# Performance work log

Measured on AMD Instinct MI355X. Metric: run time of the kernel, lower is better.

Reference implementation:

```python
import jax, jax.numpy as jnp
import numpy as np

N, E, G = 100000, 1600000, 256
F_IN, HID, NCLS = 16, 64, 2
EPS = 1e-5


def segment_mean(v, seg, num_segments):
    s = jax.ops.segment_sum(v, seg, num_segments=num_segments)
    c = jax.ops.segment_sum(jnp.ones((v.shape[0], 1), v.dtype), seg, num_segments=num_segments)
    return s / jnp.maximum(c, 1.0)


def graph_norm(x, seg, weight, bias, mean_scale):
    # PyG GraphNorm: per-graph mean/var with learnable mean_scale
    mean = segment_mean(x, seg, G)                      # [G, C]
    centered = x - mean_scale * mean[seg]               # [N, C]
    var = segment_mean(centered * centered, seg, G)     # [G, C]
    return weight * centered * jax.lax.rsqrt(var[seg] + EPS) + bias


def gcn_conv(x, W, b, row, col, n):
    # PyG GCNConv: h = x @ W; symmetric norm with added self-loops; scatter-add; + bias
    h = x @ W                                           # [N, C_out]
    deg = jnp.zeros((n,), x.dtype).at[row].add(1.0) + 1.0  # +1 self-loop
    dinv = jax.lax.rsqrt(deg)
    norm = (dinv[row] * dinv[col])[:, None]             # [E, 1]
    agg = jnp.zeros_like(h).at[row].add(norm * h[col])  # neighbor messages
    agg = agg + (dinv * dinv)[:, None] * h              # self-loop messages
    return agg + b


def setup_inputs():
    key = jax.random.key(0)
    ks = jax.random.split(key, 16)
    x = jax.random.normal(ks[0], (N, F_IN), jnp.float32)
    edge_index = jax.random.randint(ks[1], (2, E), 0, N, jnp.int32)
    batch = jnp.sort(jax.random.randint(ks[2], (N,), 0, G, jnp.int32))
    s = lambda k, shp: jax.random.normal(k, shp, jnp.float32) * 0.05
    return {
        "x": x, "edge_index": edge_index, "batch": batch,
        "gn0_w": jnp.ones((F_IN,)), "gn0_b": jnp.zeros((F_IN,)), "gn0_ms": jnp.ones((F_IN,)),
        "W1": s(ks[3], (F_IN, HID)), "b1": jnp.zeros((HID,)),
        "gn1_w": jnp.ones((HID,)), "gn1_b": jnp.zeros((HID,)), "gn1_ms": jnp.ones((HID,)),
        "W2": s(ks[4], (HID, HID)), "b2": jnp.zeros((HID,)),
        "gn2_w": jnp.ones((HID,)), "gn2_b": jnp.zeros((HID,)), "gn2_ms": jnp.ones((HID,)),
        "W3": s(ks[5], (HID, HID)), "b3": jnp.zeros((HID,)),
        "Wd": s(ks[6], (HID, HID)), "bd": jnp.zeros((HID,)),
        "Wo": s(ks[7], (HID, NCLS)), "bo": jnp.zeros((NCLS,)),
    }


def reference(x, edge_index, batch, gn0_w, gn0_b, gn0_ms, W1, b1, gn1_w, gn1_b, gn1_ms,
              W2, b2, gn2_w, gn2_b, gn2_ms, W3, b3, Wd, bd, Wo, bo):
    row, col = edge_index[0], edge_index[1]
    h = graph_norm(x, batch, gn0_w, gn0_b, gn0_ms)
    h = jax.nn.relu(gcn_conv(h, W1, b1, row, col, N))
    h = graph_norm(h, batch, gn1_w, gn1_b, gn1_ms)
    h = jax.nn.relu(gcn_conv(h, W2, b2, row, col, N))
    h = graph_norm(h, batch, gn2_w, gn2_b, gn2_ms)
    h = jax.nn.relu(gcn_conv(h, W3, b3, row, col, N))
    g = segment_mean(h, batch, G)                       # global_mean_pool -> [G, HID]
    # dropout is identity in eval mode
    g = jax.nn.relu(g @ Wd + bd)
    logits = g @ Wo + bo
    return jax.nn.softmax(logits, axis=1)
```

## Files before the change

kernel.cpp:

```cpp
#include <hip/hip_runtime.h>
#include <hip/hip_bf16.h>

#define NN 100000
#define NE 1600000
#define NG 256
#define FIN 16
#define HID 64
#define NBK 391
#define NTILE 391
#define PMAX 4864
#define BMAXP 5632
#define MAXT (NN / 16 + NG)

__device__ __forceinline__ int lower_bound_i(const int* __restrict__ b, int n, int v) {
    int lo = 0, hi = n;
    while (lo < hi) { int m = (lo + hi) >> 1; if (b[m] < v) lo = m + 1; else hi = m; }
    return lo;
}

__device__ __forceinline__ unsigned pack_bf16(float a, float b) {
    unsigned ua = __float_as_uint(a), ub = __float_as_uint(b);
    ua = (ua + 0x7fffu + ((ua >> 16) & 1u)) >> 16;
    ub = (ub + 0x7fffu + ((ub >> 16) & 1u)) & 0xffff0000u;
    return ua | ub;
}
#define BF_LO(u) __uint_as_float((u) << 16)
#define BF_HI(u) __uint_as_float((u) & 0xffff0000u)

typedef __attribute__((ext_vector_type(8))) short bf16x8;
typedef __attribute__((ext_vector_type(4))) float f32x4;
union FU { uint4 u; bf16x8 v; };

__global__ __launch_bounds__(512) void k_bhist(const int4* __restrict__ row4, int* __restrict__ bhist) {
    __shared__ int h[NBK];
    for (int i = threadIdx.x; i < NBK; i += 512) h[i] = 0;
    __syncthreads();
    int t0 = blockIdx.x * 1024 + threadIdx.x;
#pragma unroll
    for (int it = 0; it < 2; ++it) {
        int t = t0 + it * 512;
        if (t < NE / 4) {
            int4 r = row4[t];
            atomicAdd(&h[r.x >> 8], 1); atomicAdd(&h[r.y >> 8], 1);
            atomicAdd(&h[r.z >> 8], 1); atomicAdd(&h[r.w >> 8], 1);
        }
    }
    __syncthreads();
    for (int i = threadIdx.x; i < NBK; i += 512)
        if (h[i]) atomicAdd(&bhist[i], h[i]);
}

__global__ __launch_bounds__(512) void k_bscan(const int* __restrict__ bhist, int* __restrict__ bbase,
                                               int* __restrict__ bcur) {
    __shared__ int sc[512];
    int t = threadIdx.x;
    int v = (t < NBK) ? bhist[t] : 0;
    sc[t] = v;
    __syncthreads();
    int acc = v;
    for (int off = 1; off < 512; off <<= 1) {
        int add = (t >= off) ? sc[t - off] : 0;
        __syncthreads();
        acc += add;
        sc[t] = acc;
        __syncthreads();
    }
    if (t < NBK) { bbase[t] = acc - v; bcur[t] = acc - v; }
    if (t == NBK - 1) bbase[NBK] = acc;
}

__global__ __launch_bounds__(512) void k_bscatter(const int4* __restrict__ row4, const int4* __restrict__ col4,
                                                  int* __restrict__ bcur, int2* __restrict__ pairs) {
    __shared__ int lh[NBK], lofs[NBK], lbase[NBK], lc[NBK];
    __shared__ int sc[512];
    __shared__ int2 stg[4096];
    for (int i = threadIdx.x; i < NBK; i += 512) { lh[i] = 0; lc[i] = 0; }
    __syncthreads();
    int t0 = blockIdx.x * 1024 + threadIdx.x;
#pragma unroll
    for (int it = 0; it < 2; ++it) {
        int t = t0 + it * 512;
        if (t < NE / 4) {
            int4 r = row4[t];
            atomicAdd(&lh[r.x >> 8], 1); atomicAdd(&lh[r.y >> 8], 1);
            atomicAdd(&lh[r.z >> 8], 1); atomicAdd(&lh[r.w >> 8], 1);
        }
    }
    __syncthreads();
    {
        int t = threadIdx.x;
        int v = (t < NBK) ? lh[t] : 0;
        sc[t] = v;
        __syncthreads();
        int acc = v;
        for (int off = 1; off < 512; off <<= 1) {
            int add = (t >= off) ? sc[t - off] : 0;
            __syncthreads();
            acc += add;
            sc[t] = acc;
            __syncthreads();
        }
        if (t < NBK) lofs[t] = acc - v;
    }
    if (threadIdx.x < NBK) {
        int c = lh[threadIdx.x];
        lbase[threadIdx.x] = c ? atomicAdd(&bcur[threadIdx.x], c) : 0;
    }
    __syncthreads();
#pragma unroll
    for (int it = 0; it < 2; ++it) {
        int t = t0 + it * 512;
        if (t < NE / 4) {
            int4 r = row4[t];
            int4 c = col4[t];
            int b, rk;
            b = r.x >> 8; rk = atomicAdd(&lc[b], 1); stg[lofs[b] + rk] = make_int2(r.x, c.x);
            b = r.y >> 8; rk = atomicAdd(&lc[b], 1); stg[lofs[b] + rk] = make_int2(r.y, c.y);
            b = r.z >> 8; rk = atomicAdd(&lc[b], 1); stg[lofs[b] + rk] = make_int2(r.z, c.z);
            b = r.w >> 8; rk = atomicAdd(&lc[b], 1); stg[lofs[b] + rk] = make_int2(r.w, c.w);
        }
    }
    __syncthreads();
    int nv = min(4096, NE - blockIdx.x * 4096);
    for (int j = threadIdx.x; j < nv; j += 512) {
        int2 p = stg[j];
        int b = p.x >> 8;
        pairs[lbase[b] + (j - lofs[b])] = p;
    }
}

__global__ __launch_bounds__(256) void k_bsort(const int2* __restrict__ pairs, const int* __restrict__ bbase,
                                               int* __restrict__ csr_col, int* __restrict__ startv,
                                               int* __restrict__ degc, float* __restrict__ dinv) {
    __shared__ int colo[BMAXP];
    __shared__ int cnt[256], pofs[256], c2[256], sc[256];
    int b = blockIdx.x;
    int s = bbase[b];
    int n = min(bbase[b + 1] - s, PMAX);
    cnt[threadIdx.x] = 0;
    c2[threadIdx.x] = 0;
    __syncthreads();
    for (int i = threadIdx.x; i < n; i += 256)
        atomicAdd(&cnt[pairs[s + i].x & 255], 1);
    __syncthreads();
    int c = cnt[threadIdx.x];
    int pc = (c + 3) & ~3;
    {
        int t = threadIdx.x, v = pc;
        sc[t] = v;
        __syncthreads();
        int acc = v;
        for (int off = 1; off < 256; off <<= 1) {
            int add = (t >= off) ? sc[t - off] : 0;
            __syncthreads();
            acc += add;
            sc[t] = acc;
            __syncthreads();
        }
        pofs[t] = acc - v;
    }
    __syncthreads();
    int ptot = sc[255];
    for (int i = threadIdx.x; i < ptot; i += 256) colo[i] = NN;
    __syncthreads();
    for (int i = threadIdx.x; i < n; i += 256) {
        int2 p = pairs[s + i];
        int lr = p.x & 255;
        int rk = atomicAdd(&c2[lr], 1);
        colo[pofs[lr] + rk] = p.y;
    }
    __syncthreads();
    int gb = b * BMAXP;
    for (int i = threadIdx.x; i < ptot; i += 256) csr_col[gb + i] = colo[i];
    int r = (b << 8) + threadIdx.x;
    if (r < NN) {
        startv[r] = gb + pofs[threadIdx.x];
        degc[r] = pc;
        dinv[r] = rsqrtf((float)(c + 1));
    }
}

__global__ __launch_bounds__(256) void k_setup(const int* __restrict__ batch, int* __restrict__ ntot,
                                               int* __restrict__ tg, int* __restrict__ tbase,
                                               int* __restrict__ tcnt, const float* __restrict__ W1,
                                               unsigned* __restrict__ Wt1p, unsigned* __restrict__ xb,
                                               unsigned* __restrict__ h2) {
    if (blockIdx.x == 1) {
        int t = threadIdx.x;
        int j = t >> 2, kq = t & 3;
#pragma unroll
        for (int i = 0; i < 4; i++) {
            int idx = kq * 4 + i;
            int k = idx * 2;
            unsigned v = 0;
            if (k < FIN) v = pack_bf16(W1[k * 64 + j], W1[(k + 1) * 64 + j]);
            Wt1p[j * 16 + idx] = v;
        }
        if (t < 32) h2[(long)NN * 32 + t] = 0u;
        if (t < 8) xb[(long)NN * 8 + t] = 0u;
        return;
    }
    __shared__ int gst[NG + 1];
    __shared__ int sc[NG];
    int t = threadIdx.x;
    gst[t] = lower_bound_i(batch, NN, t);
    if (t == 0) gst[NG] = NN;
    __syncthreads();
    int ng = gst[t + 1] - gst[t];
    int nt = (ng + 15) >> 4;
    sc[t] = nt;
    __syncthreads();
    int acc = nt;
    for (int off = 1; off < NG; off <<= 1) {
        int add = (t >= off) ? sc[t - off] : 0;
        __syncthreads();
        acc += add;
        sc[t] = acc;
        __syncthreads();
    }
    int ofs = acc - nt;
    for (int i = 0; i < nt; i++) {
        tg[ofs + i] = t;
        tbase[ofs + i] = gst[t] + i * 16;
        tcnt[ofs + i] = min(16, ng - i * 16);
    }
    if (t == NG - 1) ntot[0] = acc;
}

__global__ __launch_bounds__(512) void k_graphnorm16(const float* __restrict__ x, const int* __restrict__ batch,
                              const float* __restrict__ w, const float* __restrict__ b,
                              const float* __restrict__ ms, const float* __restrict__ dinv,
                              unsigned* __restrict__ xb) {
    constexpr int C = FIN, NPB = 512 / C;
    __shared__ float red[NPB][C], red2[NPB][C];
    __shared__ float mm_s[C], rs_s[C];
    int g = blockIdx.x;
    int s = lower_bound_i(batch, NN, g);
    int e = lower_bound_i(batch, NN, g + 1);
    float fc = (float)max(e - s, 1);
    int c = threadIdx.x % C, slot = threadIdx.x / C;

    float a1 = 0.f, a2 = 0.f;
    for (int i = s + slot; i < e; i += NPB) { float v = x[i * C + c]; a1 += v; a2 += v * v; }
    red[slot][c] = a1;
    red2[slot][c] = a2;
    __syncthreads();
    if (threadIdx.x < C) {
        float t1 = 0.f, t2 = 0.f;
        for (int k = 0; k < NPB; k++) { t1 += red[k][threadIdx.x]; t2 += red2[k][threadIdx.x]; }
        float mean = t1 / fc;
        float mm = ms[threadIdx.x] * mean;
        float var = t2 / fc - 2.f * mm * mean + mm * mm;
        mm_s[threadIdx.x] = mm;
        rs_s[threadIdx.x] = rsqrtf(var + 1e-5f);
    }
    __syncthreads();
    float mm = mm_s[c], ww = w[c] * rs_s[c], bb = b[c];
    for (int i = s + slot; i < e; i += NPB) {
        float v = (ww * (x[i * C + c] - mm) + bb) * dinv[i];
        float partner = __shfl_xor(v, 1);
        if ((c & 1) == 0) xb[(long)i * 8 + (c >> 1)] = pack_bf16(v, partner);
    }
}

__global__ __launch_bounds__(512) void k_gnstats2(const unsigned* __restrict__ xw, const int* __restrict__ batch,
                          const float* __restrict__ w, const float* __restrict__ b,
                          const float* __restrict__ ms, const float* __restrict__ W,
                          unsigned* __restrict__ Wtp, float* __restrict__ bias2) {
    __shared__ float4 red[16][32];
    __shared__ float sA[64], sB[64];
    int g = blockIdx.x;
    int s = lower_bound_i(batch, NN, g);
    int e = lower_bound_i(batch, NN, g + 1);
    float fc = (float)max(e - s, 1);
    int cu = threadIdx.x & 31, slot = threadIdx.x >> 5;

    float s1l = 0.f, s1h = 0.f, s2l = 0.f, s2h = 0.f;
    for (int i = s + slot; i < e; i += 16) {
        unsigned u = xw[(long)i * 32 + cu];
        float lo = BF_LO(u), hi = BF_HI(u);
        s1l += lo; s1h += hi; s2l += lo * lo; s2h += hi * hi;
    }
    red[slot][cu] = make_float4(s1l, s1h, s2l, s2h);
    __syncthreads();
    if (threadIdx.x < 64) {
        int cc = threadIdx.x, iu = cc >> 1, hi = cc & 1;
        float t1 = 0.f, t2 = 0.f;
        for (int k = 0; k < 16; k++) {
            float4 v = red[k][iu];
            t1 += hi ? v.y : v.x;
            t2 += hi ? v.w : v.z;
        }
        float mean = t1 / fc;
        float mm = ms[cc] * mean;
        float var = t2 / fc - 2.f * mm * mean + mm * mm;
        float A = w[cc] * rsqrtf(var + 1e-5f);
        sA[cc] = A;
        sB[cc] = b[cc] - A * mm;
    }
    __syncthreads();
    if (threadIdx.x < 256) {
        int j = threadIdx.x >> 2, kq = threadIdx.x & 3;
        unsigned* wrow = Wtp + ((long)g * 64 + j) * 32 + kq * 8;
        float part = 0.f;
#pragma unroll
        for (int i = 0; i < 8; i++) {
            int k = kq * 16 + 2 * i;
            float w0 = W[k * 64 + j], w1 = W[(k + 1) * 64 + j];
            wrow[i] = pack_bf16(sA[k] * w0, sA[k + 1] * w1);
            part += sB[k] * w0 + sB[k + 1] * w1;
        }
        part += __shfl_xor(part, 1);
        part += __shfl_xor(part, 2);
        if (kq == 0) bias2[g * 64 + j] = part;
    }
}

__global__ __launch_bounds__(256) void k_gather16(const unsigned* __restrict__ xb, const int* __restrict__ startv,
                           const int* __restrict__ degc, const float* __restrict__ dinv,
                           const int* __restrict__ csr_col, unsigned* __restrict__ agg) {
    int wave = (blockIdx.x * blockDim.x + threadIdx.x) >> 6;
    if (wave >= NN) return;
    int lane = threadIdx.x & 63;
    unsigned p = lane & 7;
    int g = lane >> 3;
    int s = startv[wave], pcnt = degc[wave];
    float di = dinv[wave];
    float ax = 0.f, ay = 0.f;
    int k = g;
    for (; k + 8 < pcnt; k += 16) {
        unsigned c0 = (unsigned)csr_col[s + k], c1 = (unsigned)csr_col[s + k + 8];
        unsigned u0 = xb[c0 * 8u + p], u1 = xb[c1 * 8u + p];
        ax += BF_LO(u0) + BF_LO(u1);
        ay += BF_HI(u0) + BF_HI(u1);
    }
    if (k < pcnt) {
        unsigned c0 = (unsigned)csr_col[s + k];
        unsigned u0 = xb[c0 * 8u + p];
        ax += BF_LO(u0);
        ay += BF_HI(u0);
    }
    ax += __shfl_xor(ax, 8);  ay += __shfl_xor(ay, 8);
    ax += __shfl_xor(ax, 16); ay += __shfl_xor(ay, 16);
    ax += __shfl_xor(ax, 32); ay += __shfl_xor(ay, 32);
    if (g == 0) {
        unsigned u = xb[(unsigned)wave * 8u + p];
        ax = (ax + BF_LO(u)) * di;
        ay = (ay + BF_HI(u)) * di;
        agg[(long)wave * 16 + p] = pack_bf16(ax, ay);
    } else if (g == 1) {
        agg[(long)wave * 16 + 8 + p] = 0u;
    }
}

template <int KU, bool PERG, bool RELU, bool DINV>
__global__ __launch_bounds__(256) void k_gemmT(const unsigned* __restrict__ Ain, const unsigned* __restrict__ Wt,
                        const float* __restrict__ biasv, const float* __restrict__ dinv,
                        const int* __restrict__ ntot, const int* __restrict__ tg,
                        const int* __restrict__ tbase, const int* __restrict__ tcnt,
                        unsigned* __restrict__ Aout) {
    const int RW = KU * 16;
    int tix = blockIdx.x * 4 + (threadIdx.x >> 6);
    if (tix >= ntot[0]) return;
    int g = tg[tix], base = tbase[tix], n = tcnt[tix];
    int l = threadIdx.x & 63, r = l & 15, q = l >> 4;
    FU a[KU];
#pragma unroll
    for (int s = 0; s < KU; s++) {
        if (r < n) a[s].u = *(const uint4*)(Ain + (long)(base + r) * RW + s * 16 + q * 4);
        else a[s].u = make_uint4(0, 0, 0, 0);
    }
    const unsigned* wb = PERG ? (Wt + (long)g * 64 * RW) : Wt;
    f32x4 acc[4];
#pragma unroll
    for (int t = 0; t < 4; t++) {
        acc[t] = (f32x4){0.f, 0.f, 0.f, 0.f};
#pragma unroll
        for (int s = 0; s < KU; s++) {
            FU bfrag;
            bfrag.u = *(const uint4*)(wb + (long)(t * 16 + r) * RW + s * 16 + q * 4);
            acc[t] = __builtin_amdgcn_mfma_f32_16x16x32_bf16(a[s].v, bfrag.v, acc[t], 0, 0, 0);
        }
    }
    const float* bb = PERG ? (biasv + g * 64) : biasv;
    float dv[4];
#pragma unroll
    for (int e = 0; e < 4; e++) {
        int node = base + q * 4 + e;
        dv[e] = DINV ? ((node < NN) ? dinv[node] : 0.f) : 1.f;
    }
#pragma unroll
    for (int t = 0; t < 4; t++) {
        float bv = bb[t * 16 + r];
#pragma unroll
        for (int e = 0; e < 4; e++) {
            float v = acc[t][e] + bv;
            if (RELU) v = fmaxf(v, 0.f);
            if (DINV) v *= dv[e];
            float part = __shfl_xor(v, 1);
            if ((q * 4 + e) < n && (r & 1) == 0)
                Aout[(long)(base + q * 4 + e) * 32 + t * 8 + (r >> 1)] = pack_bf16(v, part);
        }
    }
}

__global__ __launch_bounds__(256) void k_gather64(const unsigned* __restrict__ h2, const int* __restrict__ startv,
                           const int* __restrict__ degc, const float* __restrict__ dinv,
                           const int* __restrict__ csr_col, const float* __restrict__ bias,
                           unsigned* __restrict__ outp) {
    int wave = (blockIdx.x * blockDim.x + threadIdx.x) >> 6;
    if (wave >= NN) return;
    int lane = threadIdx.x & 63;
    unsigned p = lane & 31;
    int g = lane >> 5;
    int s = startv[wave], pcnt = degc[wave];
    float di = dinv[wave];
    float ax = 0.f, ay = 0.f;
    if (g == 0) {
        unsigned u = h2[(unsigned)wave * 32u + p];
        ax = BF_LO(u);
        ay = BF_HI(u);
    }
    int k = g * 8;
    for (; k + 8 <= pcnt; k += 16) {
        uint4 c0 = *(const uint4*)(csr_col + s + k);
        uint4 c1 = *(const uint4*)(csr_col + s + k + 4);
        unsigned u0 = h2[c0.x * 32u + p], u1 = h2[c0.y * 32u + p],
                 u2 = h2[c0.z * 32u + p], u3 = h2[c0.w * 32u + p],
                 u4 = h2[c1.x * 32u + p], u5 = h2[c1.y * 32u + p],
                 u6 = h2[c1.z * 32u + p], u7 = h2[c1.w * 32u + p];
        ax += BF_LO(u0) + BF_LO(u1) + BF_LO(u2) + BF_LO(u3)
            + BF_LO(u4) + BF_LO(u5) + BF_LO(u6) + BF_LO(u7);
        ay += BF_HI(u0) + BF_HI(u1) + BF_HI(u2) + BF_HI(u3)
            + BF_HI(u4) + BF_HI(u5) + BF_HI(u6) + BF_HI(u7);
    }
    if (k < pcnt) {
        uint4 c0 = *(const uint4*)(csr_col + s + k);
        unsigned u0 = h2[c0.x * 32u + p], u1 = h2[c0.y * 32u + p],
                 u2 = h2[c0.z * 32u + p], u3 = h2[c0.w * 32u + p];
        ax += BF_LO(u0) + BF_LO(u1) + BF_LO(u2) + BF_LO(u3);
        ay += BF_HI(u0) + BF_HI(u1) + BF_HI(u2) + BF_HI(u3);
    }
    ax += __shfl_xor(ax, 32);
    ay += __shfl_xor(ay, 32);
    if (g == 0) {
        float2 bv = ((const float2*)bias)[p];
        float vx = fmaxf(ax * di + bv.x, 0.f);
        float vy = fmaxf(ay * di + bv.y, 0.f);
        outp[(unsigned)wave * 32u + p] = pack_bf16(vx, vy);
    }
}

__global__ __launch_bounds__(1024) void k_poolhead(const unsigned* __restrict__ xw, const int* __restrict__ batch,
                       const float* __restrict__ Wd, const float* __restrict__ bd,
                       const float* __restrict__ Wo, const float* __restrict__ bo,
                       float* __restrict__ out) {
    __shared__ float red[16][64];
    __shared__ float wds[64 * 64];
    __shared__ float gs[64];
    int g = blockIdx.x;
    int s = lower_bound_i(batch, NN, g);
    int e = lower_bound_i(batch, NN, g + 1);
    int c = threadIdx.x & 63, slot = threadIdx.x >> 6;
    for (int i = threadIdx.x; i < 64 * 64; i += 1024) wds[i] = Wd[i];
    float acc = 0.f;
    for (int i = s + slot; i < e; i += 16) {
        unsigned u = xw[(long)i * 32 + (c >> 1)];
        acc += (c & 1) ? BF_HI(u) : BF_LO(u);
    }
    red[slot][c] = acc;
    __syncthreads();
    if (threadIdx.x < 64) {
        float t = 0.f;
        for (int k = 0; k < 16; k++) t += red[k][threadIdx.x];
        gs[threadIdx.x] = t / (float)max(e - s, 1);
    }
    __syncthreads();
    if (threadIdx.x < 64) {
        int j = threadIdx.x;
        float a2 = bd[j];
        for (int k = 0; k < 64; k++) a2 += gs[k] * wds[k * 64 + j];
        float hv = fmaxf(a2, 0.f);
        float p0 = hv * Wo[j * 2 + 0], p1 = hv * Wo[j * 2 + 1];
        for (int off = 32; off; off >>= 1) { p0 += __shfl_down(p0, off); p1 += __shfl_down(p1, off); }
        if (j == 0) {
            float l0 = p0 + bo[0], l1 = p1 + bo[1];
            float m = fmaxf(l0, l1);
            float e0 = expf(l0 - m), e1 = expf(l1 - m);
            float inv = 1.f / (e0 + e1);
            out[g * 2 + 0] = e0 * inv;
            out[g * 2 + 1] = e1 * inv;
        }
    }
}

extern "C" void kernel_launch(void* const* d_in, const int* in_sizes, int n_in,
                              void* d_out, int out_size, void* d_ws, size_t ws_size,
                              hipStream_t stream) {
    const float* x = (const float*)d_in[0];
    const int* ei = (const int*)d_in[1];
    const int* row = ei;
    const int* col = ei + NE;
    const int* batch = (const int*)d_in[2];
    const float* gn0w = (const float*)d_in[3];
    const float* gn0b = (const float*)d_in[4];
    const float* gn0ms = (const float*)d_in[5];
    const float* W1 = (const float*)d_in[6];
    const float* b1 = (const float*)d_in[7];
    const float* gn1w = (const float*)d_in[8];
    const float* gn1b = (const float*)d_in[9];
    const float* gn1ms = (const float*)d_in[10];
    const float* W2 = (const float*)d_in[11];
    const float* b2 = (const float*)d_in[12];
    const float* gn2w = (const float*)d_in[13];
    const float* gn2b = (const float*)d_in[14];
    const float* gn2ms = (const float*)d_in[15];
    const float* W3 = (const float*)d_in[16];
    const float* b3 = (const float*)d_in[17];
    const float* Wd = (const float*)d_in[18];
    const float* bd = (const float*)d_in[19];
    const float* Wo = (const float*)d_in[20];
    const float* bo = (const float*)d_in[21];
    float* outp = (float*)d_out;

    int* bhist = (int*)d_ws;
    int* bbase = bhist + 512;
    int* bcur = bbase + 512;
    int* startv = bcur + 512;
    int* degc = startv + NN;
    float* dinv = (float*)(degc + NN);
    int* csr_col = (int*)(dinv + NN);
    int* ntot = csr_col + (long)NBK * BMAXP;
    int* tg = ntot + 16;
    int* tbase = tg + 6608;
    int* tcnt = tbase + 6608;
    unsigned* Wt1p = (unsigned*)(tcnt + 6608);
    unsigned* Wtp = Wt1p + 1024;
    float* bias2 = (float*)(Wtp + (long)NG * 64 * 32);
    unsigned* xb = (unsigned*)(bias2 + NG * 64);
    unsigned* agg16 = xb + (long)NN * 8 + 16;
    unsigned* bufA = agg16 + (long)NN * 16;
    unsigned* bufB = bufA + (long)NN * 32;
    unsigned* h2 = bufB + (long)NN * 32;
    int2* pairs = (int2*)bufA;

    const int NBG = (MAXT + 3) / 4;

    hipMemsetAsync(bhist, 0, 512 * sizeof(int), stream);
    k_bhist<<<NTILE, 512, 0, stream>>>((const int4*)row, bhist);
    k_bscan<<<1, 512, 0, stream>>>(bhist, bbase, bcur);
    k_bscatter<<<NTILE, 512, 0, stream>>>((const int4*)row, (const int4*)col, bcur, pairs);
    k_bsort<<<NBK, 256, 0, stream>>>(pairs, bbase, csr_col, startv, degc, dinv);

    k_setup<<<2, 256, 0, stream>>>(batch, ntot, tg, tbase, tcnt, W1, Wt1p, xb, h2);

    k_graphnorm16<<<NG, 512, 0, stream>>>(x, batch, gn0w, gn0b, gn0ms, dinv, xb);
    k_gather16<<<(NN * 64 + 255) / 256, 256, 0, stream>>>(xb, startv, degc, dinv, csr_col, agg16);
    k_gemmT<1, false, true, false><<<NBG, 256, 0, stream>>>(agg16, Wt1p, b1, dinv, ntot, tg, tbase, tcnt, bufA);

    k_gnstats2<<<NG, 512, 0, stream>>>(bufA, batch, gn1w, gn1b, gn1ms, W2, Wtp, bias2);
    k_gemmT<2, true, false, true><<<NBG, 256, 0, stream>>>(bufA, Wtp, bias2, dinv, ntot, tg, tbase, tcnt, h2);
    k_gather64<<<(NN * 64 + 255) / 256, 256, 0, stream>>>(h2, startv, degc, dinv, csr_col, b2, bufB);

    k_gnstats2<<<NG, 512, 0, stream>>>(bufB, batch, gn2w, gn2b, gn2ms, W3, Wtp, bias2);
    k_gemmT<2, true, false, true><<<NBG, 256, 0, stream>>>(bufB, Wtp, bias2, dinv, ntot, tg, tbase, tcnt, h2);
    k_gather64<<<(NN * 64 + 255) / 256, 256, 0, stream>>>(h2, startv, degc, dinv, csr_col, b3, bufA);

    k_poolhead<<<NG, 1024, 0, stream>>>(bufA, batch, Wd, bd, Wo, bo, outp);
}
```

Baseline: 382.3 us.

## Drop bucket histogram and scan passes by using fixed-capacity bucket slots

The global bucket histogram and scan kernels are removed. Each bucket now gets a fixed slot of BMAXP pairs, and k_bscatter reserves positions with an atomic counter (bcur), which k_bsort then reads as that bucket's count. This saves two kernel launches and one full read of the row array, but relies on no bucket exceeding its fixed capacity. Per-row degrees are no longer padded to multiples of four, so the 64-wide gather switches from aligned uint4 column loads to bounds-checked scalar loads.

Measured after the change: 375.9 us. About the same (-1.7%).

```diff
diff --git a/kernel.cpp b/kernel.cpp
--- a/kernel.cpp
+++ b/kernel.cpp
@@ -30,44 +30,6 @@
 typedef __attribute__((ext_vector_type(8))) short bf16x8;
 typedef __attribute__((ext_vector_type(4))) float f32x4;
 union FU { uint4 u; bf16x8 v; };
-
-__global__ __launch_bounds__(512) void k_bhist(const int4* __restrict__ row4, int* __restrict__ bhist) {
-    __shared__ int h[NBK];
-    for (int i = threadIdx.x; i < NBK; i += 512) h[i] = 0;
-    __syncthreads();
-    int t0 = blockIdx.x * 1024 + threadIdx.x;
-#pragma unroll
-    for (int it = 0; it < 2; ++it) {
-        int t = t0 + it * 512;
-        if (t < NE / 4) {
-            int4 r = row4[t];
-            atomicAdd(&h[r.x >> 8], 1); atomicAdd(&h[r.y >> 8], 1);
-            atomicAdd(&h[r.z >> 8], 1); atomicAdd(&h[r.w >> 8], 1);
-        }
-    }
-    __syncthreads();
-    for (int i = threadIdx.x; i < NBK; i += 512)
-        if (h[i]) atomicAdd(&bhist[i], h[i]);
-}
-
-__global__ __launch_bounds__(512) void k_bscan(const int* __restrict__ bhist, int* __restrict__ bbase,
-                                               int* __restrict__ bcur) {
-    __shared__ int sc[512];
-    int t = threadIdx.x;
-    int v = (t < NBK) ? bhist[t] : 0;
-    sc[t] = v;
-    __syncthreads();
-    int acc = v;
-    for (int off = 1; off < 512; off <<= 1) {
-        int add = (t >= off) ? sc[t - off] : 0;
-        __syncthreads();
-        acc += add;
-        sc[t] = acc;
-        __syncthreads();
-    }
-    if (t < NBK) { bbase[t] = acc - v; bcur[t] = acc - v; }
-    if (t == NBK - 1) bbase[NBK] = acc;
-}
 
 __global__ __launch_bounds__(512) void k_bscatter(const int4* __restrict__ row4, const int4* __restrict__ col4,
                                                   int* __restrict__ bcur, int2* __restrict__ pairs) {
@@ -125,23 +87,23 @@
     for (int j = threadIdx.x; j < nv; j += 512) {
         int2 p = stg[j];
         int b = p.x >> 8;
-        pairs[lbase[b] + (j - lofs[b])] = p;
-    }
-}
-
-__global__ __launch_bounds__(256) void k_bsort(const int2* __restrict__ pairs, const int* __restrict__ bbase,
+        pairs[(long)b * BMAXP + lbase[b] + (j - lofs[b])] = p;
+    }
+}
+
+__global__ __launch_bounds__(256) void k_bsort(const int2* __restrict__ pairs, const int* __restrict__ bcur,
                                                int* __restrict__ csr_col, int* __restrict__ startv,
                                                int* __restrict__ degc, float* __restrict__ dinv) {
     __shared__ int colo[BMAXP];
     __shared__ int cnt[256], pofs[256], c2[256], sc[256];
     int b = blockIdx.x;
-    int s = bbase[b];
-    int n = min(bbase[b + 1] - s, PMAX);
+    long sp = (long)b * BMAXP;
+    int n = min(bcur[b], PMAX);
     cnt[threadIdx.x] = 0;
     c2[threadIdx.x] = 0;
     __syncthreads();
     for (int i = threadIdx.x; i < n; i += 256)
-        atomicAdd(&cnt[pairs[s + i].x & 255], 1);
+        atomicAdd(&cnt[pairs[sp + i].x & 255], 1);
     __syncthreads();
     int c = cnt[threadIdx.x];
     int pc = (c + 3) & ~3;
@@ -164,7 +126,7 @@
     for (int i = threadIdx.x; i < ptot; i += 256) colo[i] = NN;
     __syncthreads();
     for (int i = threadIdx.x; i < n; i += 256) {
-        int2 p = pairs[s + i];
+        int2 p = pairs[sp + i];
         int lr = p.x & 255;
         int rk = atomicAdd(&c2[lr], 1);
         colo[pofs[lr] + rk] = p.y;
@@ -175,7 +137,7 @@
     int r = (b << 8) + threadIdx.x;
     if (r < NN) {
         startv[r] = gb + pofs[threadIdx.x];
-        degc[r] = pc;
+        degc[r] = c;
         dinv[r] = rsqrtf((float)(c + 1));
     }
 }
@@ -324,17 +286,17 @@
     int lane = threadIdx.x & 63;
     unsigned p = lane & 7;
     int g = lane >> 3;
-    int s = startv[wave], pcnt = degc[wave];
+    int s = startv[wave], cnt = degc[wave];
     float di = dinv[wave];
     float ax = 0.f, ay = 0.f;
     int k = g;
-    for (; k + 8 < pcnt; k += 16) {
+    for (; k + 8 < cnt; k += 16) {
         unsigned c0 = (unsigned)csr_col[s + k], c1 = (unsigned)csr_col[s + k + 8];
         unsigned u0 = xb[c0 * 8u + p], u1 = xb[c1 * 8u + p];
         ax += BF_LO(u0) + BF_LO(u1);
         ay += BF_HI(u0) + BF_HI(u1);
     }
-    if (k < pcnt) {
+    if (k < cnt) {
         unsigned c0 = (unsigned)csr_col[s + k];
         unsigned u0 = xb[c0 * 8u + p];
         ax += BF_LO(u0);
@@ -413,7 +375,7 @@
     int lane = threadIdx.x & 63;
     unsigned p = lane & 31;
     int g = lane >> 5;
-    int s = startv[wave], pcnt = degc[wave];
+    int s = startv[wave], cnt = degc[wave];
     float di = dinv[wave];
     float ax = 0.f, ay = 0.f;
     if (g == 0) {
@@ -421,25 +383,19 @@
         ax = BF_LO(u);
         ay = BF_HI(u);
     }
-    int k = g * 8;
-    for (; k + 8 <= pcnt; k += 16) {
-        uint4 c0 = *(const uint4*)(csr_col + s + k);
-        uint4 c1 = *(const uint4*)(csr_col + s + k + 4);
-        unsigned u0 = h2[c0.x * 32u + p], u1 = h2[c0.y * 32u + p],
-                 u2 = h2[c0.z * 32u + p], u3 = h2[c0.w * 32u + p],
-                 u4 = h2[c1.x * 32u + p], u5 = h2[c1.y * 32u + p],
-                 u6 = h2[c1.z * 32u + p], u7 = h2[c1.w * 32u + p];
-        ax += BF_LO(u0) + BF_LO(u1) + BF_LO(u2) + BF_LO(u3)
-            + BF_LO(u4) + BF_LO(u5) + BF_LO(u6) + BF_LO(u7);
-        ay += BF_HI(u0) + BF_HI(u1) + BF_HI(u2) + BF_HI(u3)
-            + BF_HI(u4) + BF_HI(u5) + BF_HI(u6) + BF_HI(u7);
-    }
-    if (k < pcnt) {
-        uint4 c0 = *(const uint4*)(csr_col + s + k);
-        unsigned u0 = h2[c0.x * 32u + p], u1 = h2[c0.y * 32u + p],
-                 u2 = h2[c0.z * 32u + p], u3 = h2[c0.w * 32u + p];
-        ax += BF_LO(u0) + BF_LO(u1) + BF_LO(u2) + BF_LO(u3);
-        ay += BF_HI(u0) + BF_HI(u1) + BF_HI(u2) + BF_HI(u3);
+    for (int k = g * 8; k < cnt; k += 16) {
+        int cc[8];
+#pragma unroll
+        for (int i = 0; i < 8; i++) {
+            int idx = k + i;
+            cc[i] = (idx < cnt) ? csr_col[s + idx] : -1;
+        }
+        unsigned u[8];
+#pragma unroll
+        for (int i = 0; i < 8; i++)
+            u[i] = (cc[i] >= 0) ? h2[(unsigned)cc[i] * 32u + p] : 0u;
+#pragma unroll
+        for (int i = 0; i < 8; i++) { ax += BF_LO(u[i]); ay += BF_HI(u[i]); }
     }
     ax += __shfl_xor(ax, 32);
     ay += __shfl_xor(ay, 32);
@@ -523,9 +479,7 @@
     const float* bo = (const float*)d_in[21];
     float* outp = (float*)d_out;
 
-    int* bhist = (int*)d_ws;
-    int* bbase = bhist + 512;
-    int* bcur = bbase + 512;
+    int* bcur = (int*)d_ws;
     int* startv = bcur + 512;
     int* degc = startv + NN;
     float* dinv = (float*)(degc + NN);
@@ -546,11 +500,9 @@
 
     const int NBG = (MAXT + 3) / 4;
 
-    hipMemsetAsync(bhist, 0, 512 * sizeof(int), stream);
-    k_bhist<<<NTILE, 512, 0, stream>>>((const int4*)row, bhist);
-    k_bscan<<<1, 512, 0, stream>>>(bhist, bbase, bcur);
+    hipMemsetAsync(bcur, 0, 512 * sizeof(int), stream);
     k_bscatter<<<NTILE, 512, 0, stream>>>((const int4*)row, (const int4*)col, bcur, pairs);
-    k_bsort<<<NBK, 256, 0, stream>>>(pairs, bbase, csr_col, startv, degc, dinv);
+    k_bsort<<<NBK, 256, 0, stream>>>(pairs, bcur, csr_col, startv, degc, dinv);
 
     k_setup<<<2, 256, 0, stream>>>(batch, ntot, tg, tbase, tcnt, W1, Wt1p, xb, h2);
 
```
